# Kernel optimization log

Measured on AMD Instinct MI355X. Metric: run time of the kernel, lower is better.

## Reference

```python
import jax, jax.numpy as jnp
import numpy as np
from jax import lax

K = 5  # nearest neighbors (includes self)
EPS = 1e-6


def _relu(a):
    return jnp.maximum(a, 0.0)


def setup_inputs() -> dict:
    key = jax.random.key(0)
    ks = jax.random.split(key, 16)
    B, N, D = 8, 4096, 2
    LD = 64  # local_dim

    def w(k, fan_in, fan_out):
        return jax.random.normal(k, (fan_in, fan_out), jnp.float32) / np.sqrt(fan_in)

    x = jax.random.normal(ks[0], (B, N, D), jnp.float32)
    inp = {
        "x": x,
        # local_mlp: D->64->128->LD
        "lw1": w(ks[1], D, 64), "lb1": jnp.zeros((64,), jnp.float32),
        "lw2": w(ks[2], 64, 128), "lb2": jnp.zeros((128,), jnp.float32),
        "lw3": w(ks[3], 128, LD), "lb3": jnp.zeros((LD,), jnp.float32),
        # cls_branch: (D+LD)->128->128
        "cw1": w(ks[4], D + LD, 128), "cb1": jnp.zeros((128,), jnp.float32),
        "cw2": w(ks[5], 128, 128), "cb2": jnp.zeros((128,), jnp.float32),
        # topo_branch: LD->128->128
        "tw1": w(ks[6], LD, 128), "tb1": jnp.zeros((128,), jnp.float32),
        "tw2": w(ks[7], 128, 128), "tb2": jnp.zeros((128,), jnp.float32),
    }
    return inp


def reference(x, lw1, lb1, lw2, lb2, lw3, lb3,
              cw1, cb1, cw2, cb2, tw1, tb1, tw2, tb2):
    B, N, D = x.shape
    # squared pairwise distances (B,N,N)
    sq = jnp.sum(x * x, axis=-1)
    dist_sq = sq[:, :, None] + sq[:, None, :] - 2.0 * jnp.einsum("bnd,bmd->bnm", x, x)
    _, idx = lax.top_k(-dist_sq, K)  # (B,N,K) nearest (self first)

    neighbors = x[jnp.arange(B)[:, None, None], idx]          # (B,N,K,D)
    rel = neighbors - x[:, :, None, :]                         # relative coords
    centered = rel - rel.mean(axis=2, keepdims=True)           # (B,N,K,D)
    cov = jnp.einsum("bnki,bnkj->bnij", centered, centered) / (K - 1)

    e, v = jnp.linalg.eigh(cov + EPS * jnp.eye(2, dtype=x.dtype))  # ascending eigvals
    v1 = v[..., :, 1]                                          # principal eigenvector
    base_angle = jnp.arctan2(v1[..., 1], v1[..., 0])[..., None]  # (B,N,1)

    base_axes = jnp.sqrt(jnp.maximum(e, EPS))                  # (B,N,2)
    base_axes = base_axes[..., ::-1]                           # descending: major first
    base_axes = base_axes / (base_axes.max(axis=-1, keepdims=True) + EPS)
    base_axes = jnp.maximum(base_axes, 0.2)

    lcc = jnp.einsum("bnki,bnij->bnkj", centered, v)           # canonical coords
    h = _relu(lcc @ lw1 + lb1)
    h = _relu(h @ lw2 + lb2)
    h = _relu(h @ lw3 + lb3)                                   # (B,N,K,LD)
    local_feats = h.max(axis=2)                                # (B,N,LD)

    cls_in = jnp.concatenate([x, local_feats], axis=-1)
    cls_features = _relu(_relu(cls_in @ cw1 + cb1) @ cw2 + cb2)
    topo_features = _relu(_relu(local_feats @ tw1 + tb1) @ tw2 + tb2)
    return (cls_features, topo_features, base_angle, base_axes)
```

## Files before the change

### kernel.cpp

```cpp
#include <hip/hip_runtime.h>
#include <math.h>

#pragma clang fp contract(off)

#define NPTS 4096
#define PTS  32768
#define ROWS 163840
#define QN   8
#define QLEN 512
#define SLOTS 8

#define EPS_L   5.9604644775390625e-8f
#define EPS2_L  3.5527136788005009e-15f
#define SAFMIN_L 1.1754943508222875e-38f

__device__ __forceinline__ float frn_mul(float a, float b) { float r = a * b; return r; }
__device__ __forceinline__ float frn_add(float a, float b) { float r = a + b; return r; }
__device__ __forceinline__ float frn_sub(float a, float b) { float r = a - b; return r; }
__device__ __forceinline__ float frn_div(float a, float b) { float r = a / b; return r; }

__device__ __forceinline__ float ref_sq(float x0, float x1) {
  return frn_add(frn_mul(x0, x0), frn_mul(x1, x1));
}
__device__ __forceinline__ float ref_key(float nx, float ny, float sqn,
                                         float mx, float my, float sqm) {
  float dot = fmaf(ny, my, frn_mul(nx, mx));
  float s = frn_add(sqn, sqm);
  return fmaf(-2.0f, dot, s);
}

__global__ __launch_bounds__(256) void prep_w(
    const float* __restrict__ lw1, const float* __restrict__ lw2, const float* __restrict__ lw3,
    const float* __restrict__ cw1, const float* __restrict__ cw2,
    const float* __restrict__ tw1, const float* __restrict__ tw2,
    float* __restrict__ wt) {
  const int Ks[7]   = {2, 64, 128, 66, 128, 64, 128};
  const int Kp[7]   = {2, 64, 128, 80, 128, 64, 128};
  const int Ns[7]   = {64, 128, 64, 128, 128, 128, 128};
  const int offs[7] = {0, 128, 8320, 16512, 26752, 43136, 51328};
  const float* srcs[7] = {lw1, lw2, lw3, cw1, cw2, tw1, tw2};
  int b = blockIdx.x;
  const float* src = srcs[b];
  float* dst = wt + offs[b];
  int K = Ks[b], KP = Kp[b], N = Ns[b];
  for (int e = threadIdx.x; e < KP * N; e += 256) {
    int j = e / KP, i = e - j * KP;
    dst[e] = (i < K) ? src[i * N + j] : 0.0f;
  }
}

__device__ __forceinline__ void cand_step(float mex, float mey, float cx, float cy,
                                          unsigned int idx, unsigned int T,
                                          unsigned int* sbuf, int t,
                                          unsigned int& cnt) {
  float dx = mex - cx, dy = mey - cy;
  float dist = fmaf(dy, dy, dx * dx);
  unsigned int v = (__float_as_uint(dist) & 0xFFFFF000u) | idx;
  sbuf[cnt * 128 + t] = v;
  cnt += (v < T) ? 1u : 0u;
}

__global__ __launch_bounds__(128) void knn_scan(const float* __restrict__ x,
                                                unsigned int* __restrict__ ipart) {
  __shared__ float2 cand[QLEN];
  __shared__ unsigned int sbuf[16 * 128];
  int bx = blockIdx.x;
  int q = bx & (QN - 1);
  int pg = bx >> 3;
  int batch = pg >> 5;
  const float* xb = x + (size_t)batch * NPTS * 2;
  int c0 = q * QLEN;
  for (int i = threadIdx.x; i < QLEN; i += 128)
    cand[i] = ((const float2*)xb)[c0 + i];
  __syncthreads();
  int t = threadIdx.x;
  int p = pg * 128 + t;
  float2 me = ((const float2*)x)[p];
  unsigned int d[SLOTS];
#pragma unroll
  for (int s = 0; s < SLOTS; s++) d[s] = 0xFFFFFFFFu;
  unsigned int T = 0xFFFFFFFFu;
  unsigned int cnt = 0;
  for (int mm = 0; mm < QLEN / 4; mm++) {
    float4 c01 = ((const float4*)cand)[2 * mm];
    float4 c23 = ((const float4*)cand)[2 * mm + 1];
    unsigned int idx0 = (unsigned int)(c0 + 4 * mm);
    cand_step(me.x, me.y, c01.x, c01.y, idx0 + 0u, T, sbuf, t, cnt);
    cand_step(me.x, me.y, c01.z, c01.w, idx0 + 1u, T, sbuf, t, cnt);
    cand_step(me.x, me.y, c23.x, c23.y, idx0 + 2u, T, sbuf, t, cnt);
    cand_step(me.x, me.y, c23.z, c23.w, idx0 + 3u, T, sbuf, t, cnt);
    if (__any((int)(cnt >= 13u))) {
#pragma unroll
      for (int j = 0; j < 16; j++) {
        unsigned int u = ((unsigned)j < cnt) ? sbuf[j * 128 + t] : 0xFFFFFFFFu;
#pragma unroll
        for (int s = 0; s < SLOTS; s++) {
          unsigned int lo = min(u, d[s]);
          unsigned int hi = max(u, d[s]);
          d[s] = lo; u = hi;
        }
      }
      cnt = 0;
      T = d[SLOTS - 1];
    }
  }
#pragma unroll
  for (int j = 0; j < 16; j++) {
    unsigned int u = ((unsigned)j < cnt) ? sbuf[j * 128 + t] : 0xFFFFFFFFu;
#pragma unroll
    for (int s = 0; s < SLOTS; s++) {
      unsigned int lo = min(u, d[s]);
      unsigned int hi = max(u, d[s]);
      d[s] = lo; u = hi;
    }
  }
#pragma unroll
  for (int s = 0; s < SLOTS; s++)
    ipart[((size_t)(q * SLOTS + s)) * PTS + p] = d[s];
}

#define CAS(a, b) { unsigned int _l = min(a, b), _h = max(a, b); a = _l; b = _h; }

__global__ __launch_bounds__(128) void merge_geom(const float* __restrict__ x,
    const unsigned int* __restrict__ ipart,
    float2* __restrict__ lcct2,
    float* __restrict__ angle_out, float2* __restrict__ axes_out,
    float* __restrict__ lftx) {
  int p = blockIdx.x * 128 + threadIdx.x;
  int batch = p >> 12;
  const float2* xb = (const float2*)(x + (size_t)batch * NPTS * 2);
  float2 me = ((const float2*)x)[p];
  lftx[p] = me.x;
  lftx[PTS + p] = me.y;
#pragma unroll
  for (int r = 66; r < 80; r++) lftx[(size_t)r * PTS + p] = 0.0f;
  float sqn = ref_sq(me.x, me.y);

  unsigned int g[SLOTS];
#pragma unroll
  for (int s = 0; s < SLOTS; s++) g[s] = ipart[(size_t)s * PTS + p];
  for (int qs = 1; qs < QN; qs++) {
    unsigned int B[SLOTS];
#pragma unroll
    for (int s = 0; s < SLOTS; s++) B[s] = ipart[(size_t)(qs * SLOTS + s) * PTS + p];
    unsigned int w[SLOTS];
#pragma unroll
    for (int s = 0; s < SLOTS; s++) w[s] = min(g[s], B[SLOTS - 1 - s]);
    CAS(w[0], w[4]); CAS(w[1], w[5]); CAS(w[2], w[6]); CAS(w[3], w[7]);
    CAS(w[0], w[2]); CAS(w[1], w[3]); CAS(w[4], w[6]); CAS(w[5], w[7]);
    CAS(w[0], w[1]); CAS(w[2], w[3]); CAS(w[4], w[5]); CAS(w[6], w[7]);
#pragma unroll
    for (int s = 0; s < SLOTS; s++) g[s] = w[s];
  }

  float dk[5]; int id[5];
#pragma unroll
  for (int s = 0; s < 5; s++) { dk[s] = 3.0e38f; id[s] = 0x7fffffff; }
#pragma unroll
  for (int s8 = 0; s8 < SLOTS; s8++) {
    int ci = (int)(g[s8] & 0xFFFu);
    float2 c = xb[ci];
    float key = ref_key(me.x, me.y, sqn, c.x, c.y, ref_sq(c.x, c.y));
    float v = key; int vi = ci;
#pragma unroll
    for (int s = 0; s < 5; s++) {
      bool lt = (v < dk[s]) || (v == dk[s] && vi < id[s]);
      float tv = dk[s]; int ti = id[s];
      if (lt) { dk[s] = v; id[s] = vi; v = tv; vi = ti; }
    }
  }
  float rx[5], ry[5];
  float sx = 0.f, sy = 0.f;
#pragma unroll
  for (int k = 0; k < 5; k++) {
    float2 nb = xb[id[k]];
    rx[k] = frn_sub(nb.x, me.x); ry[k] = frn_sub(nb.y, me.y);
    sx = frn_add(sx, rx[k]); sy = frn_add(sy, ry[k]);
  }
  float mx = frn_div(sx, 5.0f), my = frn_div(sy, 5.0f);
  float c00 = 0.f, c01 = 0.f, c11 = 0.f;
#pragma unroll
  for (int k = 0; k < 5; k++) {
    rx[k] = frn_sub(rx[k], mx); ry[k] = frn_sub(ry[k], my);
    c00 = frn_add(c00, frn_mul(rx[k], rx[k]));
    c01 = frn_add(c01, frn_mul(rx[k], ry[k]));
    c11 = frn_add(c11, frn_mul(ry[k], ry[k]));
  }
  c00 = frn_div(c00, 4.0f); c01 = frn_div(c01, 4.0f); c11 = frn_div(c11, 4.0f);
  float A = frn_add(c00, 1e-6f), Bv = c01, C = frn_add(c11, 1e-6f);

  float absA = fabsf(A), absC = fabsf(C), absB = fabsf(Bv);
  float thr = frn_mul(frn_mul(sqrtf(absA), sqrtf(absC)), EPS_L);
  bool diag = (absB == 0.f) || (absB <= thr);
  if (!diag) {
    bool qr = (absC < absA);
    float b2 = frn_mul(absB, absB);
    float t = qr ? frn_add(frn_mul(frn_mul(EPS2_L, absC), absA), SAFMIN_L)
                 : frn_add(frn_mul(frn_mul(EPS2_L, absA), absC), SAFMIN_L);
    if (b2 <= t) diag = true;
  }
  float e1, e2, v00, v10, v01, v11;
  if (diag) {
    if (C < A) { e1 = C; e2 = A; v00 = 0.f; v10 = 1.f; v01 = 1.f; v11 = 0.f; }
    else       { e1 = A; e2 = C; v00 = 1.f; v10 = 0.f; v01 = 0.f; v11 = 1.f; }
  } else {
    float sm = frn_add(A, C), df = frn_sub(A, C);
    float adf = fabsf(df), tb = frn_add(Bv, Bv), ab = fabsf(tb);
    float rt;
    if (adf > ab) {
      float r = frn_div(ab, adf);
      rt = frn_mul(adf, sqrtf(frn_add(1.0f, frn_mul(r, r))));
    } else if (adf < ab) {
      float r = frn_div(adf, ab);
      rt = frn_mul(ab, sqrtf(frn_add(1.0f, frn_mul(r, r))));
    } else {
      rt = frn_mul(ab, sqrtf(2.0f));
    }
    float acmx, acmn;
    if (absA > absC) { acmx = A; acmn = C; } else { acmx = C; acmn = A; }
    float rt1, rt2; int sgn1;
    if (sm < 0.f) {
      rt1 = frn_mul(0.5f, frn_sub(sm, rt)); sgn1 = -1;
      rt2 = frn_sub(frn_mul(frn_div(acmx, rt1), acmn), frn_mul(frn_div(Bv, rt1), Bv));
    } else if (sm > 0.f) {
      rt1 = frn_mul(0.5f, frn_add(sm, rt)); sgn1 = 1;
      rt2 = frn_sub(frn_mul(frn_div(acmx, rt1), acmn), frn_mul(frn_div(Bv, rt1), Bv));
    } else {
      rt1 = frn_mul(0.5f, rt); rt2 = frn_mul(-0.5f, rt); sgn1 = 1;
    }
    float cs, cs1, sn1; int sgn2;
    if (df >= 0.f) { cs = frn_add(df, rt); sgn2 = 1; }
    else           { cs = frn_sub(df, rt); sgn2 = -1; }
    float acs = fabsf(cs);
    if (acs > ab) {
      float ct = frn_div(-tb, cs);
      sn1 = frn_div(1.0f, sqrtf(frn_add(1.0f, frn_mul(ct, ct))));
      cs1 = frn_mul(ct, sn1);
    } else {
      if (ab == 0.f) { cs1 = 1.0f; sn1 = 0.0f; }
      else {
        float tn = frn_div(-cs, tb);
        cs1 = frn_div(1.0f, sqrtf(frn_add(1.0f, frn_mul(tn, tn))));
        sn1 = frn_mul(tn, cs1);
      }
    }
    if (sgn1 == sgn2) { float t = cs1; cs1 = -sn1; sn1 = t; }
    if (rt2 < rt1) { e1 = rt2; e2 = rt1; v00 = -sn1; v10 = cs1; v01 = cs1;  v11 = sn1; }
    else           { e1 = rt1; e2 = rt2; v00 = cs1;  v10 = sn1; v01 = -sn1; v11 = cs1; }
  }

  angle_out[p] = atan2f(v11, v01);
  float aM = sqrtf(fmaxf(e2, 1e-6f));
  float am = sqrtf(fmaxf(e1, 1e-6f));
  float den = frn_add(fmaxf(aM, am), 1e-6f);
  axes_out[p] = make_float2(fmaxf(frn_div(aM, den), 0.2f),
                            fmaxf(frn_div(am, den), 0.2f));

  size_t rowb = (size_t)p * 5;
#pragma unroll
  for (int k = 0; k < 5; k++) {
    float l0 = frn_add(frn_mul(rx[k], v00), frn_mul(ry[k], v10));
    float l1 = frn_add(frn_mul(rx[k], v01), frn_mul(ry[k], v11));
    lcct2[rowb + k] = make_float2(l0, l1);
  }
}

__global__ __launch_bounds__(256, 3) void gemm_l2(
    const float2* __restrict__ lcct2, const float* __restrict__ lw1t,
    const float* __restrict__ lb1,
    const float* __restrict__ wt, const float* __restrict__ bias,
    float* __restrict__ out_t, int M) {
  __shared__ float alds[16 * 128];
  __shared__ float wlds[16 * 128];
  __shared__ float w1s[192];
  int t = threadIdx.x;
  int m0 = blockIdx.x * 128;
  if (t < 192) w1s[t] = (t < 128) ? lw1t[t] : lb1[t - 128];
  int mloc = t & 127;
  int kbase = t >> 7;
  float2 lme = lcct2[m0 + mloc];
  int tm = t & 15;
  int tn = t >> 4;
  float acc[8][8];
#pragma unroll
  for (int j = 0; j < 8; j++) {
    float b = bias[tn * 8 + j];
#pragma unroll
    for (int i = 0; i < 8; i++) acc[j][i] = b;
  }
  for (int kt = 0; kt < 4; kt++) {
    int k0 = kt * 16;
    __syncthreads();
#pragma unroll
    for (int pp = 0; pp < 8; pp++) {
      int kk = pp * 2 + kbase;
      int k = k0 + kk;
      float h = fmaf(lme.y, w1s[2 * k + 1], fmaf(lme.x, w1s[2 * k], w1s[128 + k]));
      alds[kk * 128 + mloc] = fmaxf(h, 0.f);
    }
#pragma unroll
    for (int pp = 0; pp < 2; pp++) {
      int e = pp * 256 + t;
      int n = e >> 2;
      int kc = e & 3;
      float4 v = *(const float4*)(wt + (size_t)n * 64 + k0 + kc * 4);
      wlds[(kc * 4 + 0) * 128 + n] = v.x;
      wlds[(kc * 4 + 1) * 128 + n] = v.y;
      wlds[(kc * 4 + 2) * 128 + n] = v.z;
      wlds[(kc * 4 + 3) * 128 + n] = v.w;
    }
    __syncthreads();
#pragma unroll
    for (int kk = 0; kk < 16; kk++) {
      float af[8], wf[8];
      *(float4*)(af)     = *(const float4*)(alds + kk * 128 + tm * 8);
      *(float4*)(af + 4) = *(const float4*)(alds + kk * 128 + tm * 8 + 4);
      *(float4*)(wf)     = *(const float4*)(wlds + kk * 128 + tn * 8);
      *(float4*)(wf + 4) = *(const float4*)(wlds + kk * 128 + tn * 8 + 4);
#pragma unroll
      for (int j = 0; j < 8; j++)
#pragma unroll
        for (int i = 0; i < 8; i++)
          acc[j][i] = fmaf(af[i], wf[j], acc[j][i]);
    }
  }
#pragma unroll
  for (int j = 0; j < 8; j++) {
    int n = tn * 8 + j;
    float4 o0, o1;
    o0.x = fmaxf(acc[j][0], 0.f); o0.y = fmaxf(acc[j][1], 0.f);
    o0.z = fmaxf(acc[j][2], 0.f); o0.w = fmaxf(acc[j][3], 0.f);
    o1.x = fmaxf(acc[j][4], 0.f); o1.y = fmaxf(acc[j][5], 0.f);
    o1.z = fmaxf(acc[j][6], 0.f); o1.w = fmaxf(acc[j][7], 0.f);
    float* dst = out_t + (size_t)n * M + m0 + tm * 8;
    *(float4*)(dst) = o0;
    *(float4*)(dst + 4) = o1;
  }
}

__global__ __launch_bounds__(512, 4) void gemm_l3max(
    const float* __restrict__ h2, const float* __restrict__ wt,
    const float* __restrict__ bias, float* __restrict__ lftx) {
  __shared__ float alds[16 * 320];
  __shared__ float wlds[16 * 64];
  int t = threadIdx.x;
  int m0 = blockIdx.x * 320;
  int pt = t & 63;
  int ng = t >> 6;
  float acc[5][8];
#pragma unroll
  for (int j = 0; j < 8; j++) {
    float b = bias[ng * 8 + j];
#pragma unroll
    for (int r = 0; r < 5; r++) acc[r][j] = b;
  }
  for (int kt = 0; kt < 8; kt++) {
    int k0 = kt * 16;
    __syncthreads();
    for (int e = t; e < 1280; e += 512) {
      int kk = e / 80;
      int m4 = e - kk * 80;
      float4 v = *(const float4*)(h2 + (size_t)(k0 + kk) * ROWS + m0 + m4 * 4);
      *(float4*)(alds + kk * 320 + m4 * 4) = v;
    }
    if (t < 256) {
      int n = t >> 2, kc = t & 3;
      float4 v = *(const float4*)(wt + (size_t)n * 128 + k0 + kc * 4);
      wlds[(kc * 4 + 0) * 64 + n] = v.x;
      wlds[(kc * 4 + 1) * 64 + n] = v.y;
      wlds[(kc * 4 + 2) * 64 + n] = v.z;
      wlds[(kc * 4 + 3) * 64 + n] = v.w;
    }
    __syncthreads();
#pragma unroll
    for (int kk = 0; kk < 16; kk++) {
      float af[5], wf[8];
#pragma unroll
      for (int r = 0; r < 5; r++) af[r] = alds[kk * 320 + pt * 5 + r];
      *(float4*)(wf)     = *(const float4*)(wlds + kk * 64 + ng * 8);
      *(float4*)(wf + 4) = *(const float4*)(wlds + kk * 64 + ng * 8 + 4);
#pragma unroll
      for (int r = 0; r < 5; r++)
#pragma unroll
        for (int j = 0; j < 8; j++)
          acc[r][j] = fmaf(af[r], wf[j], acc[r][j]);
    }
  }
  int p = blockIdx.x * 64 + pt;
#pragma unroll
  for (int j = 0; j < 8; j++) {
    float r0 = fmaxf(acc[0][j], 0.f), r1 = fmaxf(acc[1][j], 0.f);
    float r2 = fmaxf(acc[2][j], 0.f), r3 = fmaxf(acc[3][j], 0.f);
    float r4 = fmaxf(acc[4][j], 0.f);
    float m = fmaxf(fmaxf(fmaxf(r0, r1), fmaxf(r2, r3)), r4);
    lftx[(size_t)(ng * 8 + j + 2) * PTS + p] = m;
  }
}

__global__ __launch_bounds__(512, 4) void gemm_head(
    const float* __restrict__ lftx, const float* __restrict__ wtbase,
    const float* __restrict__ cb1, const float* __restrict__ tb1,
    const float* __restrict__ cb2, const float* __restrict__ tb2,
    float* __restrict__ outbase) {
  __shared__ float a1lds[128 * 128];
  __shared__ float alds[16 * 128];
  __shared__ float wlds[16 * 128];
  int bid = blockIdx.x;
  bool isC = bid < 256;
  const float* in_t = isC ? lftx : (lftx + 2 * PTS);
  const float* w1   = isC ? (wtbase + 16512) : (wtbase + 43136);
  const float* b1   = isC ? cb1 : tb1;
  const float* w2   = isC ? (wtbase + 26752) : (wtbase + 51328);
  const float* b2   = isC ? cb2 : tb2;
  float* out        = isC ? outbase : (outbase + 4194304);
  int Kstr = isC ? 80 : 64;
  int KT   = isC ? 5 : 4;
  int m0 = (bid & 255) * 128;
  int t = threadIdx.x;
  int tm2 = t & 31;
  int tnn = t >> 5;
  int skk = t >> 5, sm4 = t & 31;
  int swn = t >> 2, swk = t & 3;
  float acc[8][4];

#pragma unroll
  for (int j = 0; j < 8; j++) {
    float b = b1[tnn * 8 + j];
#pragma unroll
    for (int i = 0; i < 4; i++) acc[j][i] = b;
  }
  for (int kt = 0; kt < KT; kt++) {
    int k0 = kt * 16;
    __syncthreads();
    {
      float4 v = *(const float4*)(in_t + (size_t)(k0 + skk) * PTS + m0 + sm4 * 4);
      *(float4*)(alds + skk * 128 + sm4 * 4) = v;
    }
    {
      float4 v = *(const float4*)(w1 + (size_t)swn * Kstr + k0 + swk * 4);
      wlds[(swk * 4 + 0) * 128 + swn] = v.x;
      wlds[(swk * 4 + 1) * 128 + swn] = v.y;
      wlds[(swk * 4 + 2) * 128 + swn] = v.z;
      wlds[(swk * 4 + 3) * 128 + swn] = v.w;
    }
    __syncthreads();
#pragma unroll
    for (int kk = 0; kk < 16; kk++) {
      float af[4], wf[8];
      *(float4*)(af)     = *(const float4*)(alds + kk * 128 + tm2 * 4);
      *(float4*)(wf)     = *(const float4*)(wlds + kk * 128 + tnn * 8);
      *(float4*)(wf + 4) = *(const float4*)(wlds + kk * 128 + tnn * 8 + 4);
#pragma unroll
      for (int j = 0; j < 8; j++)
#pragma unroll
        for (int i = 0; i < 4; i++)
          acc[j][i] = fmaf(af[i], wf[j], acc[j][i]);
    }
  }
#pragma unroll
  for (int j = 0; j < 8; j++) {
    int n = tnn * 8 + j;
    float4 o;
    o.x = fmaxf(acc[j][0], 0.f); o.y = fmaxf(acc[j][1], 0.f);
    o.z = fmaxf(acc[j][2], 0.f); o.w = fmaxf(acc[j][3], 0.f);
    *(float4*)(a1lds + n * 128 + tm2 * 4) = o;
  }

#pragma unroll
  for (int j = 0; j < 8; j++) {
    float b = b2[tnn * 8 + j];
#pragma unroll
    for (int i = 0; i < 4; i++) acc[j][i] = b;
  }
  for (int kt = 0; kt < 8; kt++) {
    int k0 = kt * 16;
    __syncthreads();
    {
      float4 v = *(const float4*)(w2 + (size_t)swn * 128 + k0 + swk * 4);
      wlds[(swk * 4 + 0) * 128 + swn] = v.x;
      wlds[(swk * 4 + 1) * 128 + swn] = v.y;
      wlds[(swk * 4 + 2) * 128 + swn] = v.z;
      wlds[(swk * 4 + 3) * 128 + swn] = v.w;
    }
    __syncthreads();
#pragma unroll
    for (int kk = 0; kk < 16; kk++) {
      float af[4], wf[8];
      *(float4*)(af)     = *(const float4*)(a1lds + (k0 + kk) * 128 + tm2 * 4);
      *(float4*)(wf)     = *(const float4*)(wlds + kk * 128 + tnn * 8);
      *(float4*)(wf + 4) = *(const float4*)(wlds + kk * 128 + tnn * 8 + 4);
#pragma unroll
      for (int j = 0; j < 8; j++)
#pragma unroll
        for (int i = 0; i < 4; i++)
          acc[j][i] = fmaf(af[i], wf[j], acc[j][i]);
    }
  }
#pragma unroll
  for (int i = 0; i < 4; i++) {
    int m = m0 + tm2 * 4 + i;
    float4 q0, q1;
    q0.x = fmaxf(acc[0][i], 0.f); q0.y = fmaxf(acc[1][i], 0.f);
    q0.z = fmaxf(acc[2][i], 0.f); q0.w = fmaxf(acc[3][i], 0.f);
    q1.x = fmaxf(acc[4][i], 0.f); q1.y = fmaxf(acc[5][i], 0.f);
    q1.z = fmaxf(acc[6][i], 0.f); q1.w = fmaxf(acc[7][i], 0.f);
    float* dst = out + (size_t)m * 128 + tnn * 8;
    *(float4*)(dst) = q0;
    *(float4*)(dst + 4) = q1;
  }
}

extern "C" void kernel_launch(void* const* d_in, const int* in_sizes, int n_in,
                              void* d_out, int out_size, void* d_ws, size_t ws_size,
                              hipStream_t stream) {
  const float* x   = (const float*)d_in[0];
  const float* lb1 = (const float*)d_in[2];
  const float* lb2 = (const float*)d_in[4];
  const float* lb3 = (const float*)d_in[6];
  const float* cb1 = (const float*)d_in[8];
  const float* cb2 = (const float*)d_in[10];
  const float* tb1 = (const float*)d_in[12];
  const float* tb2 = (const float*)d_in[14];

  float* out = (float*)d_out;
  float* angle_out = out + 8388608;
  float* axes_out  = out + 8421376;

  float* W = (float*)d_ws;
  float* wt    = W;
  float* R1    = W + 67712;
  float* R2    = R1 + 10485760;
  float* R3    = R2 + 10485760;
  float* lftx  = R3 + 20971520;
  float* lcct2 = lftx + 2621440;
  unsigned int* ipart = (unsigned int*)R1;
  float* h2    = R3;
  (void)R2;

  prep_w<<<7, 256, 0, stream>>>((const float*)d_in[1], (const float*)d_in[3], (const float*)d_in[5],
                                (const float*)d_in[7], (const float*)d_in[9],
                                (const float*)d_in[11], (const float*)d_in[13], wt);
  knn_scan<<<2048, 128, 0, stream>>>(x, ipart);
  merge_geom<<<256, 128, 0, stream>>>(x, ipart, (float2*)lcct2, angle_out, (float2*)axes_out, lftx);

  gemm_l2<<<ROWS / 128, 256, 0, stream>>>((const float2*)lcct2, wt + 0, lb1,
                                          wt + 128, lb2, h2, ROWS);
  gemm_l3max<<<PTS / 64, 512, 0, stream>>>(h2, wt + 8320, lb3, lftx);

  gemm_head<<<512, 512, 0, stream>>>(lftx, wt, cb1, tb1, cb2, tb2, out);
}
```

Baseline: 287.9 us.

## Fuse local MLP layers 2 and 3 with max-pool into one kernel

Merges the layer-2 GEMM and the layer-3 GEMM plus max-over-neighbors kernel into a single kernel. Layer-2 output is computed in two 64-channel halves and kept in LDS, then consumed by layer 3 immediately. This avoids writing and re-reading the 128 x 163840 h2 intermediate in global memory and saves a launch. In exchange it uses a large LDS footprint per block (about 120 KB), allowing fewer resident blocks, and the layer-1 activations are recomputed for each half.

```diff
diff --git a/kernel.cpp b/kernel.cpp
--- a/kernel.cpp
+++ b/kernel.cpp
@@ -265,135 +265,124 @@
   }
 }
 
-__global__ __launch_bounds__(256, 3) void gemm_l2(
+__global__ __launch_bounds__(512, 2) void gemm_l23max(
     const float2* __restrict__ lcct2, const float* __restrict__ lw1t,
     const float* __restrict__ lb1,
-    const float* __restrict__ wt, const float* __restrict__ bias,
-    float* __restrict__ out_t, int M) {
-  __shared__ float alds[16 * 128];
-  __shared__ float wlds[16 * 128];
+    const float* __restrict__ w2g, const float* __restrict__ lb2,
+    const float* __restrict__ w3g, const float* __restrict__ lb3,
+    float* __restrict__ lftx) {
+  __shared__ float h2lds[64 * 320];
+  __shared__ float alds[16 * 320];
+  __shared__ float w2lds[64 * 64];
+  __shared__ float w3lds[64 * 64];
   __shared__ float w1s[192];
   int t = threadIdx.x;
-  int m0 = blockIdx.x * 128;
+  int m0 = blockIdx.x * 320;
+  int p0 = blockIdx.x * 64;
+  int pt = t & 63;
+  int fg = t >> 6;
+  int sn = t & 63, skq = t >> 6;
   if (t < 192) w1s[t] = (t < 128) ? lw1t[t] : lb1[t - 128];
-  int mloc = t & 127;
-  int kbase = t >> 7;
-  float2 lme = lcct2[m0 + mloc];
-  int tm = t & 15;
-  int tn = t >> 4;
-  float acc[8][8];
+
+  float acc3[8][5];
 #pragma unroll
   for (int j = 0; j < 8; j++) {
-    float b = bias[tn * 8 + j];
-#pragma unroll
-    for (int i = 0; i < 8; i++) acc[j][i] = b;
-  }
-  for (int kt = 0; kt < 4; kt++) {
-    int k0 = kt * 16;
+    float b = lb3[fg * 8 + j];
+#pragma unroll
+    for (int r = 0; r < 5; r++) acc3[j][r] = b;
+  }
+
+  for (int half = 0; half < 2; half++) {
     __syncthreads();
-#pragma unroll
-    for (int pp = 0; pp < 8; pp++) {
-      int kk = pp * 2 + kbase;
-      int k = k0 + kk;
-      float h = fmaf(lme.y, w1s[2 * k + 1], fmaf(lme.x, w1s[2 * k], w1s[128 + k]));
-      alds[kk * 128 + mloc] = fmaxf(h, 0.f);
-    }
-#pragma unroll
-    for (int pp = 0; pp < 2; pp++) {
-      int e = pp * 256 + t;
-      int n = e >> 2;
-      int kc = e & 3;
-      float4 v = *(const float4*)(wt + (size_t)n * 64 + k0 + kc * 4);
-      wlds[(kc * 4 + 0) * 128 + n] = v.x;
-      wlds[(kc * 4 + 1) * 128 + n] = v.y;
-      wlds[(kc * 4 + 2) * 128 + n] = v.z;
-      wlds[(kc * 4 + 3) * 128 + n] = v.w;
+    {
+      const float* src = w2g + (size_t)(half * 64 + sn) * 64 + skq * 8;
+      float4 v0 = *(const float4*)(src);
+      float4 v1 = *(const float4*)(src + 4);
+      w2lds[(skq * 8 + 0) * 64 + sn] = v0.x;
+      w2lds[(skq * 8 + 1) * 64 + sn] = v0.y;
+      w2lds[(skq * 8 + 2) * 64 + sn] = v0.z;
+      w2lds[(skq * 8 + 3) * 64 + sn] = v0.w;
+      w2lds[(skq * 8 + 4) * 64 + sn] = v1.x;
+      w2lds[(skq * 8 + 5) * 64 + sn] = v1.y;
+      w2lds[(skq * 8 + 6) * 64 + sn] = v1.z;
+      w2lds[(skq * 8 + 7) * 64 + sn] = v1.w;
+    }
+    float acc2[8][5];
+#pragma unroll
+    for (int j = 0; j < 8; j++) {
+      float b = lb2[half * 64 + fg * 8 + j];
+#pragma unroll
+      for (int r = 0; r < 5; r++) acc2[j][r] = b;
+    }
+    for (int kt = 0; kt < 4; kt++) {
+      __syncthreads();
+#pragma unroll
+      for (int pass = 0; pass < 10; pass++) {
+        int e = pass * 512 + t;
+        int kk = e / 320;
+        int m = e - kk * 320;
+        int k = kt * 16 + kk;
+        float2 l = lcct2[m0 + m];
+        float h = fmaf(l.y, w1s[2 * k + 1], fmaf(l.x, w1s[2 * k], w1s[128 + k]));
+        alds[kk * 320 + m] = fmaxf(h, 0.f);
+      }
+      __syncthreads();
+#pragma unroll
+      for (int kk = 0; kk < 16; kk++) {
+        int k = kt * 16 + kk;
+        float af[5], wf[8];
+#pragma unroll
+        for (int r = 0; r < 5; r++) af[r] = alds[kk * 320 + pt * 5 + r];
+        *(float4*)(wf)     = *(const float4*)(w2lds + k * 64 + fg * 8);
+        *(float4*)(wf + 4) = *(const float4*)(w2lds + k * 64 + fg * 8 + 4);
+#pragma unroll
+        for (int j = 0; j < 8; j++)
+#pragma unroll
+          for (int r = 0; r < 5; r++)
+            acc2[j][r] = fmaf(af[r], wf[j], acc2[j][r]);
+      }
+    }
+#pragma unroll
+    for (int j = 0; j < 8; j++)
+#pragma unroll
+      for (int r = 0; r < 5; r++)
+        h2lds[(fg * 8 + j) * 320 + pt * 5 + r] = fmaxf(acc2[j][r], 0.f);
+    {
+      const float* src = w3g + (size_t)sn * 128 + half * 64 + skq * 8;
+      float4 v0 = *(const float4*)(src);
+      float4 v1 = *(const float4*)(src + 4);
+      w3lds[(skq * 8 + 0) * 64 + sn] = v0.x;
+      w3lds[(skq * 8 + 1) * 64 + sn] = v0.y;
+      w3lds[(skq * 8 + 2) * 64 + sn] = v0.z;
+      w3lds[(skq * 8 + 3) * 64 + sn] = v0.w;
+      w3lds[(skq * 8 + 4) * 64 + sn] = v1.x;
+      w3lds[(skq * 8 + 5) * 64 + sn] = v1.y;
+      w3lds[(skq * 8 + 6) * 64 + sn] = v1.z;
+      w3lds[(skq * 8 + 7) * 64 + sn] = v1.w;
     }
     __syncthreads();
-#pragma unroll
-    for (int kk = 0; kk < 16; kk++) {
-      float af[8], wf[8];
-      *(float4*)(af)     = *(const float4*)(alds + kk * 128 + tm * 8);
-      *(float4*)(af + 4) = *(const float4*)(alds + kk * 128 + tm * 8 + 4);
-      *(float4*)(wf)     = *(const float4*)(wlds + kk * 128 + tn * 8);
-      *(float4*)(wf + 4) = *(const float4*)(wlds + kk * 128 + tn * 8 + 4);
+#pragma unroll 4
+    for (int kk = 0; kk < 64; kk++) {
+      float af[5], wf[8];
+#pragma unroll
+      for (int r = 0; r < 5; r++) af[r] = h2lds[kk * 320 + pt * 5 + r];
+      *(float4*)(wf)     = *(const float4*)(w3lds + kk * 64 + fg * 8);
+      *(float4*)(wf + 4) = *(const float4*)(w3lds + kk * 64 + fg * 8 + 4);
 #pragma unroll
       for (int j = 0; j < 8; j++)
 #pragma unroll
-        for (int i = 0; i < 8; i++)
-          acc[j][i] = fmaf(af[i], wf[j], acc[j][i]);
-    }
-  }
+        for (int r = 0; r < 5; r++)
+          acc3[j][r] = fmaf(af[r], wf[j], acc3[j][r]);
+    }
+  }
+  int p = p0 + pt;
 #pragma unroll
   for (int j = 0; j < 8; j++) {
-    int n = tn * 8 + j;
-    float4 o0, o1;
-    o0.x = fmaxf(acc[j][0], 0.f); o0.y = fmaxf(acc[j][1], 0.f);
-    o0.z = fmaxf(acc[j][2], 0.f); o0.w = fmaxf(acc[j][3], 0.f);
-    o1.x = fmaxf(acc[j][4], 0.f); o1.y = fmaxf(acc[j][5], 0.f);
-    o1.z = fmaxf(acc[j][6], 0.f); o1.w = fmaxf(acc[j][7], 0.f);
-    float* dst = out_t + (size_t)n * M + m0 + tm * 8;
-    *(float4*)(dst) = o0;
-    *(float4*)(dst + 4) = o1;
-  }
-}
-
-__global__ __launch_bounds__(512, 4) void gemm_l3max(
-    const float* __restrict__ h2, const float* __restrict__ wt,
-    const float* __restrict__ bias, float* __restrict__ lftx) {
-  __shared__ float alds[16 * 320];
-  __shared__ float wlds[16 * 64];
-  int t = threadIdx.x;
-  int m0 = blockIdx.x * 320;
-  int pt = t & 63;
-  int ng = t >> 6;
-  float acc[5][8];
-#pragma unroll
-  for (int j = 0; j < 8; j++) {
-    float b = bias[ng * 8 + j];
-#pragma unroll
-    for (int r = 0; r < 5; r++) acc[r][j] = b;
-  }
-  for (int kt = 0; kt < 8; kt++) {
-    int k0 = kt * 16;
-    __syncthreads();
-    for (int e = t; e < 1280; e += 512) {
-      int kk = e / 80;
-      int m4 = e - kk * 80;
-      float4 v = *(const float4*)(h2 + (size_t)(k0 + kk) * ROWS + m0 + m4 * 4);
-      *(float4*)(alds + kk * 320 + m4 * 4) = v;
-    }
-    if (t < 256) {
-      int n = t >> 2, kc = t & 3;
-      float4 v = *(const float4*)(wt + (size_t)n * 128 + k0 + kc * 4);
-      wlds[(kc * 4 + 0) * 64 + n] = v.x;
-      wlds[(kc * 4 + 1) * 64 + n] = v.y;
-      wlds[(kc * 4 + 2) * 64 + n] = v.z;
-      wlds[(kc * 4 + 3) * 64 + n] = v.w;
-    }
-    __syncthreads();
-#pragma unroll
-    for (int kk = 0; kk < 16; kk++) {
-      float af[5], wf[8];
-#pragma unroll
-      for (int r = 0; r < 5; r++) af[r] = alds[kk * 320 + pt * 5 + r];
-      *(float4*)(wf)     = *(const float4*)(wlds + kk * 64 + ng * 8);
-      *(float4*)(wf + 4) = *(const float4*)(wlds + kk * 64 + ng * 8 + 4);
-#pragma unroll
-      for (int r = 0; r < 5; r++)
-#pragma unroll
-        for (int j = 0; j < 8; j++)
-          acc[r][j] = fmaf(af[r], wf[j], acc[r][j]);
-    }
-  }
-  int p = blockIdx.x * 64 + pt;
-#pragma unroll
-  for (int j = 0; j < 8; j++) {
-    float r0 = fmaxf(acc[0][j], 0.f), r1 = fmaxf(acc[1][j], 0.f);
-    float r2 = fmaxf(acc[2][j], 0.f), r3 = fmaxf(acc[3][j], 0.f);
-    float r4 = fmaxf(acc[4][j], 0.f);
+    float r0 = fmaxf(acc3[j][0], 0.f), r1 = fmaxf(acc3[j][1], 0.f);
+    float r2 = fmaxf(acc3[j][2], 0.f), r3 = fmaxf(acc3[j][3], 0.f);
+    float r4 = fmaxf(acc3[j][4], 0.f);
     float m = fmaxf(fmaxf(fmaxf(r0, r1), fmaxf(r2, r3)), r4);
-    lftx[(size_t)(ng * 8 + j + 2) * PTS + p] = m;
+    lftx[(size_t)(fg * 8 + j + 2) * PTS + p] = m;
   }
 }
 
@@ -529,13 +518,10 @@
   float* W = (float*)d_ws;
   float* wt    = W;
   float* R1    = W + 67712;
-  float* R2    = R1 + 10485760;
-  float* R3    = R2 + 10485760;
+  float* R3    = R1 + 10485760 + 10485760;
   float* lftx  = R3 + 20971520;
   float* lcct2 = lftx + 2621440;
   unsigned int* ipart = (unsigned int*)R1;
-  float* h2    = R3;
-  (void)R2;
 
   prep_w<<<7, 256, 0, stream>>>((const float*)d_in[1], (const float*)d_in[3], (const float*)d_in[5],
                                 (const float*)d_in[7], (const float*)d_in[9],
@@ -543,9 +529,8 @@
   knn_scan<<<2048, 128, 0, stream>>>(x, ipart);
   merge_geom<<<256, 128, 0, stream>>>(x, ipart, (float2*)lcct2, angle_out, (float2*)axes_out, lftx);
 
-  gemm_l2<<<ROWS / 128, 256, 0, stream>>>((const float2*)lcct2, wt + 0, lb1,
-                                          wt + 128, lb2, h2, ROWS);
-  gemm_l3max<<<PTS / 64, 512, 0, stream>>>(h2, wt + 8320, lb3, lftx);
+  gemm_l23max<<<512, 512, 0, stream>>>((const float2*)lcct2, wt + 0, lb1,
+                                       wt + 128, lb2, wt + 8320, lb3, lftx);
 
   gemm_head<<<512, 512, 0, stream>>>(lftx, wt, cb1, tb1, cb2, tb2, out);
 }
```

Result: slower. 318.6 us (+10.7%).
